# Optimization experiments

Measured on AMD Instinct MI355X. Metric: run time of the kernel, lower is better.

Reference implementation:

```python
import jax, jax.numpy as jnp
import numpy as np

H = 16  # number of heads (init kwarg h)

def vdp_matmul(a, va, b, vb):
    # VDP propagation through a matmul of two independent Gaussian tensors:
    # mean = a @ b ; var = va @ vb + va @ b^2 + a^2 @ vb
    mu = jnp.matmul(a, b)
    var = jnp.matmul(va, vb) + jnp.matmul(va, b * b) + jnp.matmul(a * a, vb)
    return mu, var

def softmax_vdp(a, va):
    # diagonal-Jacobian VDP softmax: p = softmax(a); var = (p(1-p))^2 * va
    p = jax.nn.softmax(a, axis=-1)
    return p, (p * (1.0 - p)) ** 2 * va

def setup_inputs() -> dict:
    key = jax.random.key(0)
    ks = jax.random.split(key, 8)
    B, S, D = 2, 1024, 1024
    sc = 1.0 / np.sqrt(D)
    return {
        "x": jax.random.normal(ks[0], (B, S, D), jnp.float32),
        "var_x": jax.random.uniform(ks[1], (B, S, D), jnp.float32) * 0.1,
        "wq_mu": jax.random.normal(ks[2], (D, D), jnp.float32) * sc,
        "wq_var": jax.random.uniform(ks[3], (D, D), jnp.float32) * 0.01,
        "wk_mu": jax.random.normal(ks[4], (D, D), jnp.float32) * sc,
        "wk_var": jax.random.uniform(ks[5], (D, D), jnp.float32) * 0.01,
        "wv_mu": jax.random.normal(ks[6], (D, D), jnp.float32) * sc,
        "wv_var": jax.random.uniform(ks[7], (D, D), jnp.float32) * 0.01,
    }

def _split_heads(t, h):
    B, S, D = t.shape
    return t.reshape(B, S, h, D // h).transpose(0, 2, 1, 3)  # [B,h,S,dh]

def reference(x, var_x, wq_mu, wq_var, wk_mu, wk_var, wv_mu, wv_var):
    D = x.shape[-1]
    rd = jnp.sqrt(jnp.asarray(D, x.dtype))
    # LinearVDP (bias=False): treat weight^T as the second VDP matmul operand
    q, vq = vdp_matmul(x, var_x, wq_mu.T, wq_var.T)
    k, vk = vdp_matmul(x, var_x, wk_mu.T, wk_var.T)
    v, vv = vdp_matmul(x, var_x, wv_mu.T, wv_var.T)
    q, vq = _split_heads(q, H), _split_heads(vq, H)
    k, vk = _split_heads(k, H), _split_heads(vk, H)
    v, vv = _split_heads(v, H), _split_heads(vv, H)
    # scores: q @ k^T with VDP variance, scaled (masking=False path)
    a, va = vdp_matmul(q, vq, k.transpose(0, 1, 3, 2), vk.transpose(0, 1, 3, 2))
    a, va = a / rd, va / (rd * rd)
    a, va = softmax_vdp(a, va)
    # attention-weighted values with VDP variance
    a, va = vdp_matmul(a, va, v, vv)
    a = a.transpose(0, 2, 1, 3).reshape(x.shape)      # [B,S,D]
    va = va.transpose(0, 2, 1, 3).reshape(x.shape)    # [B,S,D]
    return x + a, va
```

## Files before the change

### kernel.cpp

```cpp
#include <hip/hip_runtime.h>
#include <stdint.h>

typedef unsigned short u16;
typedef __attribute__((ext_vector_type(4))) float f32x4;
typedef __attribute__((ext_vector_type(8))) short s16x8;
typedef __attribute__((ext_vector_type(2))) unsigned u32x2;

#define MFMA16(a,b,c) __builtin_amdgcn_mfma_f32_16x16x32_bf16(a,b,c,0,0,0)

__device__ inline u16 f2b(float f){
  unsigned u = __float_as_uint(f);
  unsigned r = u + 0x7fffu + ((u>>16)&1u);
  return (u16)(r>>16);
}
__device__ inline float b2f(u16 b){
  return __uint_as_float(((unsigned)b)<<16);
}
__device__ inline unsigned cvtpk(float lo, float hi){
  unsigned r;
  asm("v_cvt_pk_bf16_f32 %0, %1, %2" : "=v"(r) : "v"(lo), "v"(hi));
  return r;
}
__device__ inline void load_lds16(const void* g, void* l){
  __builtin_amdgcn_global_load_lds((const __attribute__((address_space(1))) void*)g,
                                   (__attribute__((address_space(3))) void*)l, 16, 0, 0);
}

__global__ void prep_in_kernel(const float* __restrict__ x, const float* __restrict__ vx,
                               const float* __restrict__ w0mu, const float* __restrict__ w0va,
                               const float* __restrict__ w1mu, const float* __restrict__ w1va,
                               const float* __restrict__ w2mu, const float* __restrict__ w2va,
                               u16* __restrict__ xb, u16* __restrict__ acat,
                               u16* __restrict__ wmub, u16* __restrict__ bcat){
  int bid = blockIdx.x;
  if (bid < 8192){
    int i = bid*256 + threadIdx.x;
    int j = i & 1023;
    float xv = x[i];
    xb[i] = f2b(xv);
    size_t ar = (size_t)(i >> 10)*2048;
    acat[ar + j]        = f2b(vx[i]);
    acat[ar + 1024 + j] = f2b(xv*xv);
  } else {
    int t = bid - 8192;
    int z = t >> 12;
    int i = (t & 4095)*256 + threadIdx.x;
    const float* wmu = z==0?w0mu:(z==1?w1mu:w2mu);
    const float* wva = z==0?w0va:(z==1?w1va:w2va);
    u16* wb = wmub + (size_t)z*1048576;
    u16* bc = bcat + (size_t)z*2097152;
    int j = i & 1023;
    float mu = wmu[i], va = wva[i];
    wb[i] = f2b(mu);
    size_t br = (size_t)(i >> 10)*2048;
    bc[br + j]        = f2b(va + mu*mu);
    bc[br + 1024 + j] = f2b(va);
  }
}

__global__ __launch_bounds__(256) void gemm_nt6_kernel(
    const u16* __restrict__ xb, const u16* __restrict__ acat,
    const u16* __restrict__ wmub, const u16* __restrict__ bcat,
    u16* __restrict__ cbase){
  int bid = blockIdx.x;
  int z = bid % 6;
  int xy = bid / 6;
  int bx = xy & 15, by = xy >> 4;
  const u16* A = z<3 ? xb : acat;
  int K = z<3 ? 1024 : 2048;
  const u16* B = z<3 ? wmub + (size_t)z*1048576 : bcat + (size_t)(z-3)*2097152;
  u16* C = cbase + (size_t)z*2097152;
  const int N = 1024;
  __shared__ __align__(16) u16 As[128*64];
  __shared__ __align__(16) u16 Bs[128*64];
  int tid = threadIdx.x;
  int wid = tid>>6, lane = tid&63;
  int wr = wid>>1, wc = wid&1;
  int fr = lane&15, kg = lane>>4;
  int m0 = bx*128, n0 = by*128;
  int srow = lane>>3;
  int sci  = (lane&7) ^ srow;
  f32x4 acc[4][4] = {};
  for (int k0=0; k0<K; k0+=64){
    #pragma unroll
    for (int cc=0; cc<4; cc++){
      int c = wid*4 + cc;
      size_t gra = (size_t)(m0 + c*8 + srow)*K + k0 + sci*8;
      size_t grb = (size_t)(n0 + c*8 + srow)*K + k0 + sci*8;
      load_lds16(A + gra, (char*)As + c*1024);
      load_lds16(B + grb, (char*)Bs + c*1024);
    }
    __syncthreads();
    #pragma unroll
    for (int kf=0;kf<2;kf++){
      s16x8 af[4], bfv[4];
      #pragma unroll
      for (int i=0;i<4;i++){
        int Ra = wr*64 + i*16 + fr;
        int Rb = wc*64 + i*16 + fr;
        af[i]  = *(const s16x8*)(As + Ra*64 + (((kg + kf*4) ^ (Ra&7))<<3));
        bfv[i] = *(const s16x8*)(Bs + Rb*64 + (((kg + kf*4) ^ (Rb&7))<<3));
      }
      #pragma unroll
      for (int i=0;i<4;i++)
        #pragma unroll
        for (int j=0;j<4;j++)
          acc[i][j] = MFMA16(bfv[j], af[i], acc[i][j]);
    }
    __syncthreads();
  }
  #pragma unroll
  for (int i=0;i<4;i++){
    int mrow = m0 + wr*64 + i*16 + fr;
    #pragma unroll
    for (int j=0;j<4;j++){
      int ncol = n0 + wc*64 + j*16 + kg*4;
      u32x2 pk = {cvtpk(acc[i][j][0],acc[i][j][1]), cvtpk(acc[i][j][2],acc[i][j][3])};
      *(u32x2*)(C + (size_t)mrow*N + ncol) = pk;
    }
  }
}

__global__ void mid_kernel(const u16* __restrict__ kb, const u16* __restrict__ vkb,
                           u16* __restrict__ kw2,
                           const u16* __restrict__ vb, const u16* __restrict__ vvb,
                           u16* __restrict__ vT, u16* __restrict__ vw2T,
                           u16* __restrict__ vvT){
  __shared__ u16 t[32][33];
  int bid = blockIdx.x;
  if (bid < 6144){
    int z = bid / 2048, wI = bid % 2048;
    int bx = wI & 31, by = wI >> 5;
    u16* out = z==0?vT:(z==1?vw2T:vvT);
    int tx = threadIdx.x & 31, ty = threadIdx.x >> 5;
    int c0 = bx*32, r0 = by*32;
    #pragma unroll
    for (int rr=0; rr<32; rr+=8){
      size_t idx = (size_t)(r0+ty+rr)*1024 + c0+tx;
      u16 val;
      if (z==0)      val = vb[idx];
      else if (z==2) val = vvb[idx];
      else {
        float v  = b2f(vb[idx]);
        float vv = b2f(vvb[idx]);
        val = f2b(vv + v*v);
      }
      t[ty+rr][tx] = val;
    }
    __syncthreads();
    #pragma unroll
    for (int rr=0; rr<32; rr+=8)
      out[(size_t)(c0+ty+rr)*2048 + r0+tx] = t[tx][ty+rr];
  } else {
    int i = (bid - 6144)*256 + threadIdx.x;
    float kk = b2f(kb[i]);
    float vk = b2f(vkb[i]);
    kw2[i] = f2b(vk + kk*kk);
  }
}

__global__ __launch_bounds__(256) void attn_vdp_kernel(
  const u16* __restrict__ qb, const u16* __restrict__ vqb,
  const u16* __restrict__ kb, const u16* __restrict__ kw2, const u16* __restrict__ vkb,
  const u16* __restrict__ vT, const u16* __restrict__ vw2T, const u16* __restrict__ vvT,
  const float* __restrict__ x, float* __restrict__ out0, float* __restrict__ out1){
  int qblk = blockIdx.x, h = blockIdx.y, b = blockIdx.z;
  int wid = threadIdx.x>>6, lane = threadIdx.x&63;
  int fr = lane&15, kg = lane>>4;
  int qrow0 = qblk*64 + wid*16;
  size_t mbase = (size_t)b*1024;

  __shared__ __align__(16) u16 bufA[3][4096];
  __shared__ __align__(16) u16 bufB[3][4096];
  __shared__ __align__(16) u16 plds[4][3][16][72];

  const int srow = lane>>3;
  const int sci  = (lane&7) ^ srow;
  const int c0   = wid*2;

  auto stA1 = [&](int jt, u16* dst){
    size_t base = (mbase + (size_t)jt*64)*1024 + h*64;
    #pragma unroll
    for (int c2=0;c2<2;c2++){
      int c = c0+c2;
      size_t go = base + (size_t)(c*8+srow)*1024 + sci*8;
      load_lds16(kb + go, (char*)dst + c*1024);
    }
  };
  auto stK3 = [&](int jt){
    size_t base = (mbase + (size_t)jt*64)*1024 + h*64;
    #pragma unroll
    for (int c2=0;c2<2;c2++){
      int c = c0+c2;
      size_t go = base + (size_t)(c*8+srow)*1024 + sci*8;
      load_lds16(kb  + go, (char*)bufA[0] + c*1024);
      load_lds16(kw2 + go, (char*)bufA[1] + c*1024);
      load_lds16(vkb + go, (char*)bufA[2] + c*1024);
    }
  };
  auto stV3 = [&](int jt){
    size_t base = (size_t)(h*64)*2048 + mbase + (size_t)jt*64;
    #pragma unroll
    for (int c2=0;c2<2;c2++){
      int c = c0+c2;
      size_t go = base + (size_t)(c*8+srow)*2048 + sci*8;
      load_lds16(vT   + go, (char*)bufB[0] + c*1024);
      load_lds16(vw2T + go, (char*)bufB[1] + c*1024);
      load_lds16(vvT  + go, (char*)bufB[2] + c*1024);
    }
  };
  auto frag = [&](const u16* t, int ni, int kf)->s16x8{
    int R = ni*16+fr;
    return *(const s16x8*)(t + R*64 + (((kg + kf*4) ^ (R&7))<<3));
  };

  s16x8 qa[2], vqa[2], qsa[2];
  {
    size_t ro = (mbase + qrow0 + fr)*1024 + h*64 + kg*8;
    #pragma unroll
    for (int kf=0;kf<2;kf++){
      qa[kf]  = *(const s16x8*)(qb  + ro + kf*32);
      vqa[kf] = *(const s16x8*)(vqb + ro + kf*32);
      #pragma unroll
      for (int e=0;e<8;e+=2){
        float lo = b2f((u16)qa[kf][e]);
        float hi = b2f((u16)qa[kf][e+1]);
        unsigned pk = cvtpk(lo*lo, hi*hi);
        qsa[kf][e]   = (short)(pk & 0xffffu);
        qsa[kf][e+1] = (short)(pk >> 16);
      }
    }
  }
  const float scale = 0.03125f;

  float lsum = 0.f;
  stA1(0, bufA[0]);
  __syncthreads();
  for (int jt=0;jt<16;jt++){
    const u16* cur = (jt&1) ? bufB[0] : bufA[0];
    if (jt<15) stA1(jt+1, (jt&1) ? bufA[0] : bufB[0]);
    else       stK3(0);
    f32x4 sacc[4] = {};
    #pragma unroll
    for (int ni=0;ni<4;ni++)
      #pragma unroll
      for (int kf=0;kf<2;kf++)
        sacc[ni] = MFMA16(frag(cur,ni,kf), qa[kf], sacc[ni]);
    #pragma unroll
    for (int ni=0;ni<4;ni++)
      #pragma unroll
      for (int r=0;r<4;r++)
        lsum += __expf(sacc[ni][r]*scale);
    __syncthreads();
  }
  lsum += __shfl_xor(lsum, 16);
  lsum += __shfl_xor(lsum, 32);
  const float linv = 1.f/lsum;

  f32x4 omu[4] = {}, ova[4] = {};
  for (int jt=0;jt<16;jt++){
    stV3(jt);
    f32x4 sacc[4] = {}, vacc[4] = {};
    #pragma unroll
    for (int ni=0;ni<4;ni++)
      #pragma unroll
      for (int kf=0;kf<2;kf++){
        sacc[ni] = MFMA16(frag(bufA[0],ni,kf), qa[kf],  sacc[ni]);
        vacc[ni] = MFMA16(frag(bufA[1],ni,kf), vqa[kf], vacc[ni]);
        vacc[ni] = MFMA16(frag(bufA[2],ni,kf), qsa[kf], vacc[ni]);
      }
    #pragma unroll
    for (int ni=0;ni<4;ni++){
      float pv[4], vpv[4], psv[4];
      #pragma unroll
      for (int r=0;r<4;r++){
        float p  = __expf(sacc[ni][r]*scale) * linv;
        float va = vacc[ni][r] * 9.765625e-4f;
        float g  = p*(1.f-p);
        pv[r]  = p;
        vpv[r] = g*g*va;
        psv[r] = p*p;
      }
      *(u32x2*)&plds[wid][0][fr][ni*16+kg*4] = (u32x2){cvtpk(pv[0],pv[1]),   cvtpk(pv[2],pv[3])};
      *(u32x2*)&plds[wid][1][fr][ni*16+kg*4] = (u32x2){cvtpk(vpv[0],vpv[1]), cvtpk(vpv[2],vpv[3])};
      *(u32x2*)&plds[wid][2][fr][ni*16+kg*4] = (u32x2){cvtpk(psv[0],psv[1]), cvtpk(psv[2],psv[3])};
    }
    s16x8 pa[2], vpa[2], pqa[2];
    #pragma unroll
    for (int kf=0;kf<2;kf++){
      pa[kf]  = *(const s16x8*)&plds[wid][0][fr][kf*32 + kg*8];
      vpa[kf] = *(const s16x8*)&plds[wid][1][fr][kf*32 + kg*8];
      pqa[kf] = *(const s16x8*)&plds[wid][2][fr][kf*32 + kg*8];
    }
    __syncthreads();
    if (jt<15) stK3(jt+1);
    #pragma unroll
    for (int ni=0;ni<4;ni++)
      #pragma unroll
      for (int kf=0;kf<2;kf++){
        omu[ni] = MFMA16(pa[kf],  frag(bufB[0],ni,kf), omu[ni]);
        ova[ni] = MFMA16(vpa[kf], frag(bufB[1],ni,kf), ova[ni]);
        ova[ni] = MFMA16(pqa[kf], frag(bufB[2],ni,kf), ova[ni]);
      }
    __syncthreads();
  }

  #pragma unroll
  for (int ni=0;ni<4;ni++){
    #pragma unroll
    for (int r=0;r<4;r++){
      size_t idx = (mbase + qrow0 + kg*4 + r)*1024 + h*64 + ni*16 + fr;
      out0[idx] = x[idx] + omu[ni][r];
      out1[idx] = ova[ni][r];
    }
  }
}

extern "C" void kernel_launch(void* const* d_in, const int* in_sizes, int n_in,
                              void* d_out, int out_size, void* d_ws, size_t ws_size,
                              hipStream_t stream){
  const float* x    = (const float*)d_in[0];
  const float* vx   = (const float*)d_in[1];
  const float* wqmu = (const float*)d_in[2];
  const float* wqva = (const float*)d_in[3];
  const float* wkmu = (const float*)d_in[4];
  const float* wkva = (const float*)d_in[5];
  const float* wvmu = (const float*)d_in[6];
  const float* wvva = (const float*)d_in[7];
  float* out0 = (float*)d_out;
  float* out1 = out0 + 2u*1024u*1024u;

  char* w = (char*)d_ws;
  const size_t MB = 1024*1024;
  u16* xb   = (u16*)(w +  0*MB);
  u16* acat = (u16*)(w +  4*MB);
  u16* wmub = (u16*)(w + 12*MB);
  u16* bcat = (u16*)(w + 18*MB);
  u16* qb_  = (u16*)(w + 30*MB);
  u16* kb_  = (u16*)(w + 34*MB);
  u16* vb_  = (u16*)(w + 38*MB);
  u16* vqb  = (u16*)(w + 42*MB);
  u16* vkb  = (u16*)(w + 46*MB);
  u16* vvb  = (u16*)(w + 50*MB);
  u16* kw2  = (u16*)(w + 54*MB);
  u16* vT   = (u16*)(w + 58*MB);
  u16* vw2T = (u16*)(w + 62*MB);
  u16* vvT  = (u16*)(w + 66*MB);

  prep_in_kernel<<<20480, 256, 0, stream>>>(x, vx, wqmu, wqva, wkmu, wkva, wvmu, wvva,
                                            xb, acat, wmub, bcat);
  gemm_nt6_kernel<<<768, 256, 0, stream>>>(xb, acat, wmub, bcat, qb_);
  mid_kernel<<<14336, 256, 0, stream>>>(kb_, vkb, kw2, vb_, vvb, vT, vw2T, vvT);
  attn_vdp_kernel<<<dim3(16,16,2), 256, 0, stream>>>(qb_, vqb, kb_, kw2, vkb,
                                                     vT, vw2T, vvT, x, out0, out1);
}
```

Before: 239.2 us.

## Double-buffer GEMM LDS tiles and raise wave priority around attention MFMAs

After: 214.4 us. 10.4% less time.

```diff
diff --git a/kernel.cpp b/kernel.cpp
--- a/kernel.cpp
+++ b/kernel.cpp
@@ -62,52 +62,50 @@
     const u16* __restrict__ xb, const u16* __restrict__ acat,
     const u16* __restrict__ wmub, const u16* __restrict__ bcat,
     u16* __restrict__ cbase){
-  int bid = blockIdx.x;
-  int z = bid % 6;
-  int xy = bid / 6;
-  int bx = xy & 15, by = xy >> 4;
+  int z = blockIdx.z;
   const u16* A = z<3 ? xb : acat;
   int K = z<3 ? 1024 : 2048;
   const u16* B = z<3 ? wmub + (size_t)z*1048576 : bcat + (size_t)(z-3)*2097152;
   u16* C = cbase + (size_t)z*2097152;
   const int N = 1024;
-  __shared__ __align__(16) u16 As[128*64];
-  __shared__ __align__(16) u16 Bs[128*64];
+  __shared__ __align__(16) u16 As[2][128*32];
+  __shared__ __align__(16) u16 Bs[2][128*32];
   int tid = threadIdx.x;
   int wid = tid>>6, lane = tid&63;
   int wr = wid>>1, wc = wid&1;
   int fr = lane&15, kg = lane>>4;
-  int m0 = bx*128, n0 = by*128;
-  int srow = lane>>3;
-  int sci  = (lane&7) ^ srow;
+  int m0 = blockIdx.x*128, n0 = blockIdx.y*128;
+  int srow = lane>>2;
+  int scol = (lane&3)*8;
+
+  auto stage = [&](int buf, int k0){
+    #pragma unroll
+    for (int c=0;c<2;c++){
+      int r = c*64 + wid*16 + srow;
+      load_lds16(A + (size_t)(m0+r)*K + k0 + scol, (char*)As[buf] + (size_t)(c*64+wid*16)*64);
+      load_lds16(B + (size_t)(n0+r)*K + k0 + scol, (char*)Bs[buf] + (size_t)(c*64+wid*16)*64);
+    }
+  };
+
   f32x4 acc[4][4] = {};
-  for (int k0=0; k0<K; k0+=64){
-    #pragma unroll
-    for (int cc=0; cc<4; cc++){
-      int c = wid*4 + cc;
-      size_t gra = (size_t)(m0 + c*8 + srow)*K + k0 + sci*8;
-      size_t grb = (size_t)(n0 + c*8 + srow)*K + k0 + sci*8;
-      load_lds16(A + gra, (char*)As + c*1024);
-      load_lds16(B + grb, (char*)Bs + c*1024);
-    }
-    __syncthreads();
-    #pragma unroll
-    for (int kf=0;kf<2;kf++){
-      s16x8 af[4], bfv[4];
-      #pragma unroll
-      for (int i=0;i<4;i++){
-        int Ra = wr*64 + i*16 + fr;
-        int Rb = wc*64 + i*16 + fr;
-        af[i]  = *(const s16x8*)(As + Ra*64 + (((kg + kf*4) ^ (Ra&7))<<3));
-        bfv[i] = *(const s16x8*)(Bs + Rb*64 + (((kg + kf*4) ^ (Rb&7))<<3));
-      }
-      #pragma unroll
-      for (int i=0;i<4;i++)
-        #pragma unroll
-        for (int j=0;j<4;j++)
-          acc[i][j] = MFMA16(bfv[j], af[i], acc[i][j]);
-    }
-    __syncthreads();
+  stage(0, 0);
+  __syncthreads();
+  int cur = 0;
+  for (int k0=0; k0<K; k0+=32){
+    if (k0+32<K) stage(cur^1, k0+32);
+    s16x8 af[4], bfv[4];
+    #pragma unroll
+    for (int i=0;i<4;i++){
+      af[i]  = *(const s16x8*)(As[cur] + (wr*64 + i*16 + fr)*32 + kg*8);
+      bfv[i] = *(const s16x8*)(Bs[cur] + (wc*64 + i*16 + fr)*32 + kg*8);
+    }
+    #pragma unroll
+    for (int i=0;i<4;i++)
+      #pragma unroll
+      for (int j=0;j<4;j++)
+        acc[i][j] = MFMA16(bfv[j], af[i], acc[i][j]);
+    __syncthreads();
+    cur ^= 1;
   }
   #pragma unroll
   for (int i=0;i<4;i++){
@@ -241,11 +239,13 @@
     if (jt<15) stA1(jt+1, (jt&1) ? bufA[0] : bufB[0]);
     else       stK3(0);
     f32x4 sacc[4] = {};
+    __builtin_amdgcn_s_setprio(1);
     #pragma unroll
     for (int ni=0;ni<4;ni++)
       #pragma unroll
       for (int kf=0;kf<2;kf++)
         sacc[ni] = MFMA16(frag(cur,ni,kf), qa[kf], sacc[ni]);
+    __builtin_amdgcn_s_setprio(0);
     #pragma unroll
     for (int ni=0;ni<4;ni++)
       #pragma unroll
@@ -261,6 +261,7 @@
   for (int jt=0;jt<16;jt++){
     stV3(jt);
     f32x4 sacc[4] = {}, vacc[4] = {};
+    __builtin_amdgcn_s_setprio(1);
     #pragma unroll
     for (int ni=0;ni<4;ni++)
       #pragma unroll
@@ -269,6 +270,7 @@
         vacc[ni] = MFMA16(frag(bufA[1],ni,kf), vqa[kf], vacc[ni]);
         vacc[ni] = MFMA16(frag(bufA[2],ni,kf), qsa[kf], vacc[ni]);
       }
+    __builtin_amdgcn_s_setprio(0);
     #pragma unroll
     for (int ni=0;ni<4;ni++){
       float pv[4], vpv[4], psv[4];
@@ -294,6 +296,7 @@
     }
     __syncthreads();
     if (jt<15) stK3(jt+1);
+    __builtin_amdgcn_s_setprio(1);
     #pragma unroll
     for (int ni=0;ni<4;ni++)
       #pragma unroll
@@ -302,6 +305,7 @@
         ova[ni] = MFMA16(vpa[kf], frag(bufB[1],ni,kf), ova[ni]);
         ova[ni] = MFMA16(pqa[kf], frag(bufB[2],ni,kf), ova[ni]);
       }
+    __builtin_amdgcn_s_setprio(0);
     __syncthreads();
   }
 
@@ -349,7 +353,7 @@
 
   prep_in_kernel<<<20480, 256, 0, stream>>>(x, vx, wqmu, wqva, wkmu, wkva, wvmu, wvva,
                                             xb, acat, wmub, bcat);
-  gemm_nt6_kernel<<<768, 256, 0, stream>>>(xb, acat, wmub, bcat, qb_);
+  gemm_nt6_kernel<<<dim3(16,8,6), 256, 0, stream>>>(xb, acat, wmub, bcat, qb_);
   mid_kernel<<<14336, 256, 0, stream>>>(kb_, vkb, kw2, vb_, vvb, vT, vw2T, vvT);
   attn_vdp_kernel<<<dim3(16,16,2), 256, 0, stream>>>(qb_, vqb, kb_, kw2, vkb,
                                                      vT, vw2T, vvT, x, out0, out1);
```
